# Optimization experiments

Measured on AMD Instinct MI355X. Metric: run time of the kernel, lower is better.

The kernel has to match this reference:

```python
import jax, jax.numpy as jnp
import numpy as np

B, H, L, N = 16, 128, 4096, 64
DT_MIN, DT_MAX = 0.001, 0.1


def _make_dplr_hippo(n):
    # NPLR HiPPO -> DPLR diagonalization (numpy, init-time only)
    p0 = np.sqrt(1 + 2 * np.arange(n))
    A = p0[:, None] * p0[None, :]
    A = -(np.tril(A) - np.diag(np.arange(n)))
    p = np.sqrt(np.arange(n) + 0.5)
    b = np.sqrt(2 * np.arange(n) + 1.0)
    S = A + p[:, None] * p[None, :]
    Lam_re = np.mean(np.diagonal(S)) * np.ones(n)
    Lam_im, V = np.linalg.eigh(S * -1j)
    p = V.conj().T @ p
    b = V.conj().T @ b
    return Lam_re + 1j * Lam_im, p, b


def setup_inputs() -> dict:
    key = jax.random.key(0)
    k1, k2, k3 = jax.random.split(key, 3)
    Lam, p, b = _make_dplr_hippo(N)
    tile = lambda a: jnp.tile(jnp.asarray(a, jnp.float32)[None], (H, 1))
    Lambda_re = tile(Lam.real)
    Lambda_im = tile(Lam.imag)
    P_ri = jnp.tile(jnp.stack([jnp.asarray(p.real, jnp.float32), jnp.asarray(p.imag, jnp.float32)], -1)[None], (H, 1, 1))
    B_ri = jnp.tile(jnp.stack([jnp.asarray(b.real, jnp.float32), jnp.asarray(b.imag, jnp.float32)], -1)[None], (H, 1, 1))
    C = (0.5 ** 0.5) * jax.random.normal(k1, (H, N, 2), jnp.float32)
    log_step = jax.random.uniform(k2, (H,)) * (np.log(DT_MAX) - np.log(DT_MIN)) + np.log(DT_MIN)
    D = jnp.ones((H,), jnp.float32)
    u = jax.random.normal(k3, (B, H, L), jnp.float32)
    return {"u": u, "Lambda_re": Lambda_re, "Lambda_im": Lambda_im, "P_ri": P_ri,
            "B_ri": B_ri, "C": C, "log_step": log_step.astype(jnp.float32), "D": D}


def reference(u, Lambda_re, Lambda_im, P_ri, B_ri, C, log_step, D):
    Lseq = u.shape[-1]
    # setup(): Lambda = clip(Lambda_re, max=-1e-4) + i*Lambda_im ; C complex ; step = exp(log_step)
    Lam = jnp.minimum(Lambda_re, -1e-4) + 1j * Lambda_im            # [H,N]
    P = P_ri[..., 0] + 1j * P_ri[..., 1]                             # [H,N]
    Bm = B_ri[..., 0] + 1j * B_ri[..., 1]                            # [H,N]
    Cc = C[..., 0] + 1j * C[..., 1]                                  # [H,N]
    step = jnp.exp(log_step)                                         # [H]
    # kernel_DPLR at the roots of unity
    Omega = jnp.exp(-2j * jnp.pi * (jnp.arange(Lseq) / Lseq))        # [L]
    g = (2.0 / step)[:, None] * ((1.0 - Omega) / (1.0 + Omega))[None, :]  # [H,L]
    c = 2.0 / (1.0 + Omega)                                          # [L]
    den = 1.0 / (g[:, :, None] - Lam[:, None, :])                    # [H,L,N] resolvent
    # four Cauchy dot products, batched: v stacked on last axis
    Vmat = jnp.stack([Cc.conj() * Bm, Cc.conj() * P, P.conj() * Bm, P.conj() * P], axis=-1)  # [H,N,4]
    Ks = jnp.einsum('hln,hnk->hlk', den, Vmat)                       # [H,L,4]
    k00, k01, k10, k11 = Ks[..., 0], Ks[..., 1], Ks[..., 2], Ks[..., 3]
    atRoots = c[None, :] * (k00 - k01 * (1.0 / (1.0 + k11)) * k10)   # [H,L]
    K = jnp.fft.ifft(atRoots, Lseq, axis=-1).real                    # [H,L] SSM kernel
    # causal FFT convolution: pad both to 2L
    ud = jnp.fft.rfft(jnp.pad(u, ((0, 0), (0, 0), (0, Lseq))), axis=-1)   # [B,H,L+1]
    Kd = jnp.fft.rfft(jnp.pad(K, ((0, 0), (0, Lseq))), axis=-1)           # [H,L+1]
    y = jnp.fft.irfft(ud * Kd[None], axis=-1)[..., :Lseq]            # [B,H,L]
    return y + D[None, :, None] * u
```

## Files before the change

kernel.cpp:

```cpp
#include <hip/hip_runtime.h>
#include <hip/hip_bf16.h>


#define PI_F 3.14159265358979323846f

__device__ __forceinline__ float2 cmulf(float2 a, float2 b) {
  return make_float2(a.x * b.x - a.y * b.y, a.x * b.y + a.y * b.x);
}
__device__ __forceinline__ void cmul_set(float2& v, float wr, float wi) {
  v = make_float2(v.x * wr - v.y * wi, v.x * wi + v.y * wr);
}
__device__ __forceinline__ int ad(int k) { return k + (k >> 4); }

template <int SIGN>
__device__ __forceinline__ void bfly4(float2& a, float2& b, float2& c,
                                      float2& d) {
  float t0x = a.x + c.x, t0y = a.y + c.y;
  float t1x = a.x - c.x, t1y = a.y - c.y;
  float t2x = b.x + d.x, t2y = b.y + d.y;
  float t3x = b.x - d.x, t3y = b.y - d.y;
  a = make_float2(t0x + t2x, t0y + t2y);
  c = make_float2(t0x - t2x, t0y - t2y);
  if (SIGN < 0) {
    b = make_float2(t1x + t3y, t1y - t3x);
    d = make_float2(t1x - t3y, t1y + t3x);
  } else {
    b = make_float2(t1x - t3y, t1y + t3x);
    d = make_float2(t1x + t3y, t1y - t3x);
  }
}

template <int SIGN>
__device__ __forceinline__ void fft16(float2 v[16]) {
  const float sg = (float)SIGN;
  const float C1 = 0.92387953251128674f;
  const float S1 = 0.38268343236508978f;
  const float R2 = 0.70710678118654752f;
  bfly4<SIGN>(v[0], v[4], v[8], v[12]);
  bfly4<SIGN>(v[1], v[5], v[9], v[13]);
  bfly4<SIGN>(v[2], v[6], v[10], v[14]);
  bfly4<SIGN>(v[3], v[7], v[11], v[15]);
  cmul_set(v[5], C1, sg * S1);
  cmul_set(v[6], R2, sg * R2);
  cmul_set(v[7], S1, sg * C1);
  cmul_set(v[9], R2, sg * R2);
  v[10] = make_float2(-sg * v[10].y, sg * v[10].x);
  cmul_set(v[11], -R2, sg * R2);
  cmul_set(v[13], S1, sg * C1);
  cmul_set(v[14], -R2, sg * R2);
  cmul_set(v[15], -C1, -sg * S1);
  float2 w[16];
#pragma unroll
  for (int g = 0; g < 4; ++g) {
    float2 x0 = v[4 * g], x1 = v[4 * g + 1], x2 = v[4 * g + 2],
           x3 = v[4 * g + 3];
    bfly4<SIGN>(x0, x1, x2, x3);
    w[g] = x0; w[g + 4] = x1; w[g + 8] = x2; w[g + 12] = x3;
  }
#pragma unroll
  for (int i = 0; i < 16; ++i) v[i] = w[i];
}

template <int SIGN>
__device__ void fft4096_regs(float2 v[16], float2* lds, int tid) {
  const float TH1 = (float)SIGN * (2.0f * PI_F / 4096.0f);
  const float TH2 = (float)SIGN * (2.0f * PI_F / 256.0f);
  fft16<SIGN>(v);
  {
    float sn, cn;
    __sincosf(TH1 * (float)tid, &sn, &cn);
    float2 w1 = make_float2(cn, sn), cw = w1;
#pragma unroll
    for (int g = 1; g < 16; ++g) {
      v[g] = cmulf(v[g], cw);
      if (g < 15) cw = cmulf(cw, w1);
    }
  }
  __syncthreads();
#pragma unroll
  for (int g = 0; g < 16; ++g) lds[tid * 17 + g] = v[g];
  __syncthreads();
  const int a = tid & 15, g2 = tid >> 4;
#pragma unroll
  for (int b = 0; b < 16; ++b) v[b] = lds[a * 17 + b * 272 + g2];
  fft16<SIGN>(v);
  {
    float sn, cn;
    __sincosf(TH2 * (float)a, &sn, &cn);
    float2 w1 = make_float2(cn, sn), cw = w1;
#pragma unroll
    for (int b = 1; b < 16; ++b) {
      v[b] = cmulf(v[b], cw);
      if (b < 15) cw = cmulf(cw, w1);
    }
  }
  __syncthreads();
#pragma unroll
  for (int b = 0; b < 16; ++b) lds[g2 * 17 + b * 273 + a] = v[b];
  __syncthreads();
#pragma unroll
  for (int a2 = 0; a2 < 16; ++a2) v[a2] = lds[g2 * 17 + a * 273 + a2];
  fft16<SIGN>(v);
}

__global__ __launch_bounds__(256) void k_cauchy(
    const float* __restrict__ Lre, const float* __restrict__ Lim,
    const float* __restrict__ Pri, const float* __restrict__ Bri,
    const float* __restrict__ Cri, const float* __restrict__ lstep,
    float2* __restrict__ atR) {
  __shared__ float4 pA[64];
  __shared__ float4 pB[64];
  __shared__ float2 pL[64];
  const int h = blockIdx.x >> 2;
  const int sub = blockIdx.x & 3;
  const int tid = threadIdx.x;
  if (tid < 64) {
    int n = tid;
    int base = h * 64 + n;
    float lr = fminf(Lre[base], -1e-4f);
    float li = Lim[base];
    float pr = Pri[2 * base], pi = Pri[2 * base + 1];
    float br = Bri[2 * base], bi = Bri[2 * base + 1];
    float cr = Cri[2 * base], ci = Cri[2 * base + 1];
    pA[n] = make_float4(cr * br + ci * bi, cr * bi - ci * br,
                        cr * pr + ci * pi, cr * pi - ci * pr);
    pB[n] = make_float4(pr * br + pi * bi, pr * bi - pi * br,
                        pr * pr + pi * pi, 0.f);
    pL[n] = make_float2(lr, li);
  }
  __syncthreads();
  const float istep = expf(-lstep[h]);

  float trm[4], tim[4], qrm[4], qim[4];
#pragma unroll
  for (int i = 0; i < 4; ++i) {
    int m = sub * 1024 + i * 256 + tid;
    float ang = -(2.0f * PI_F / 4096.0f) * (float)m;
    float sn, cn;
    __sincosf(ang, &sn, &cn);
    trm[i] = 0.5f * (1.0f + cn);
    tim[i] = 0.5f * sn;
    qrm[i] = (1.0f - cn) * istep;
    qim[i] = -sn * istep;
  }
  float S[4][8];
#pragma unroll
  for (int i = 0; i < 4; ++i)
#pragma unroll
    for (int jj = 0; jj < 8; ++jj) S[i][jj] = 0.f;

#pragma unroll 4
  for (int n = 0; n < 64; ++n) {
    float4 a = pA[n];
    float4 b = pB[n];
    float2 L = pL[n];
#pragma unroll
    for (int i = 0; i < 4; ++i) {
      float dr = qrm[i] - (trm[i] * L.x - tim[i] * L.y);
      float di = qim[i] - (trm[i] * L.y + tim[i] * L.x);
      float inv = __builtin_amdgcn_rcpf(dr * dr + di * di);
      float sr = dr * inv, si = -di * inv;
      S[i][0] += a.x * sr - a.y * si;  S[i][1] += a.x * si + a.y * sr;
      S[i][2] += a.z * sr - a.w * si;  S[i][3] += a.z * si + a.w * sr;
      S[i][4] += b.x * sr - b.y * si;  S[i][5] += b.x * si + b.y * sr;
      S[i][6] += b.z * sr;             S[i][7] += b.z * si;
    }
  }
#pragma unroll
  for (int i = 0; i < 4; ++i) {
    int m = sub * 1024 + i * 256 + tid;
    float tS11r = trm[i] * S[i][6] - tim[i] * S[i][7];
    float tS11i = trm[i] * S[i][7] + tim[i] * S[i][6];
    float denr = 1.0f + tS11r, deni = tS11i;
    float dinv = 1.0f / (denr * denr + deni * deni);
    float P1r = S[i][2] * S[i][4] - S[i][3] * S[i][5];
    float P1i = S[i][2] * S[i][5] + S[i][3] * S[i][4];
    float P2r = trm[i] * P1r - tim[i] * P1i;
    float P2i = trm[i] * P1i + tim[i] * P1r;
    float Qr = (P2r * denr + P2i * deni) * dinv;
    float Qi = (P2i * denr - P2r * deni) * dinv;
    atR[h * 4096 + m] = make_float2(S[i][0] - Qr, S[i][1] - Qi);
  }
}

__global__ __launch_bounds__(256) void k_khat(const float2* __restrict__ atR,
                                              const float* __restrict__ Dp,
                                              float2* __restrict__ Khat) {
  __shared__ float2 lds[4368];
  const int h = blockIdx.x;
  const int tid = threadIdx.x;
  float2 v[16];
#pragma unroll
  for (int c = 0; c < 16; ++c) v[c] = atR[h * 4096 + tid + 256 * c];
  fft4096_regs<1>(v, lds, tid);
  const int kb = (tid >> 4) + 16 * (tid & 15);
  float* ldsf = (float*)lds;
  const float s = 1.0f / 4096.0f;
  __syncthreads();
#pragma unroll
  for (int al = 0; al < 16; ++al) {
    int l = kb + 256 * al;
    ldsf[ad(l)] = v[al].x * s;
  }
  __syncthreads();
#pragma unroll
  for (int c = 0; c < 8; ++c) {
    int n = tid + 256 * c;
    v[c] = make_float2(ldsf[ad(2 * n)], ldsf[ad(2 * n + 1)]);
  }
#pragma unroll
  for (int c = 8; c < 16; ++c) v[c] = make_float2(0.f, 0.f);
  fft4096_regs<-1>(v, lds, tid);
  __syncthreads();
#pragma unroll
  for (int al = 0; al < 16; ++al) {
    int k = kb + 256 * al;
    lds[ad(k)] = v[al];
  }
  __syncthreads();
  const float Dh = Dp[h];
  float2* Kr = Khat + h * 4097;
  for (int k = tid; k <= 2048; k += 256) {
    float2 Zk = lds[ad(k)];
    float2 Zm = lds[ad((4096 - k) & 4095)];
    float Er = 0.5f * (Zk.x + Zm.x), Ei = 0.5f * (Zk.y - Zm.y);
    float Or = 0.5f * (Zk.y + Zm.y), Oi = 0.5f * (Zm.x - Zk.x);
    float swn, cwn;
    __sincosf(-(PI_F / 4096.0f) * (float)k, &swn, &cwn);
    float WOr = cwn * Or - swn * Oi, WOi = cwn * Oi + swn * Or;
    Kr[k] = make_float2(Er + WOr + Dh, Ei + WOi);
    if (k != 2048) Kr[4096 - k] = make_float2(Er - WOr + Dh, WOi - Ei);
  }
}

__global__ __launch_bounds__(256) void k_conv(const float* __restrict__ u,
                                              const float2* __restrict__ Khat,
                                              float* __restrict__ y) {
  __shared__ float2 lds[4368];
  const int r = blockIdx.x;
  const int h = r & 127;
  const int tid = threadIdx.x;
  const float2* u2 = (const float2*)(u + (size_t)r * 4096);
  float2 v[16];
#pragma unroll
  for (int c = 0; c < 8; ++c) v[c] = u2[tid + 256 * c];
#pragma unroll
  for (int c = 8; c < 16; ++c) v[c] = make_float2(0.f, 0.f);
  fft4096_regs<-1>(v, lds, tid);
  const int kb = (tid >> 4) + 16 * (tid & 15);
  __syncthreads();
#pragma unroll
  for (int al = 0; al < 16; ++al) {
    int k = kb + 256 * al;
    lds[ad(k)] = v[al];
  }
  __syncthreads();
  const float2* __restrict__ Kr = Khat + h * 4097;
  const float s = 1.0f / 4096.0f;
  for (int k = tid; k <= 2048; k += 256) {
    float2 Zk = lds[ad(k)];
    float2 Zm = lds[ad((4096 - k) & 4095)];
    float Er = 0.5f * (Zk.x + Zm.x), Ei = 0.5f * (Zk.y - Zm.y);
    float Or = 0.5f * (Zk.y + Zm.y), Oi = 0.5f * (Zm.x - Zk.x);
    float swn, cwn;
    __sincosf(-(PI_F / 4096.0f) * (float)k, &swn, &cwn);
    float WOr = cwn * Or - swn * Oi, WOi = cwn * Oi + swn * Or;
    float U1r = Er + WOr, U1i = Ei + WOi;
    float U2r = Er - WOr, U2i = WOi - Ei;
    float2 K1 = Kr[k], K2 = Kr[4096 - k];
    float Y1r = U1r * K1.x - U1i * K1.y, Y1i = U1r * K1.y + U1i * K1.x;
    float Y2r = U2r * K2.x - U2i * K2.y, Y2i = U2r * K2.y + U2i * K2.x;
    float Epr = 0.5f * (Y1r + Y2r), Epi = 0.5f * (Y1i - Y2i);
    float Tr = 0.5f * (Y1r - Y2r), Ti = 0.5f * (Y1i + Y2i);
    float O2r = cwn * Tr + swn * Ti, O2i = cwn * Ti - swn * Tr;
    lds[ad(k)] = make_float2((Epr - O2i) * s, (Epi + O2r) * s);
    if (k != 0 && k != 2048)
      lds[ad(4096 - k)] = make_float2((Epr + O2i) * s, (O2r - Epi) * s);
  }
  __syncthreads();
#pragma unroll
  for (int c = 0; c < 16; ++c) {
    int j = tid + 256 * c;
    v[c] = lds[ad(j)];
  }
  fft4096_regs<1>(v, lds, tid);
  __syncthreads();
#pragma unroll
  for (int al = 0; al < 8; ++al) {
    int k = kb + 256 * al;
    lds[ad(k)] = v[al];
  }
  __syncthreads();
  float4* y4 = (float4*)(y + (size_t)r * 4096);
#pragma unroll
  for (int i = 0; i < 4; ++i) {
    int j4 = tid + 256 * i;
    float2 z0 = lds[ad(2 * j4)];
    float2 z1 = lds[ad(2 * j4 + 1)];
    y4[j4] = make_float4(z0.x, z0.y, z1.x, z1.y);
  }
}

extern "C" void kernel_launch(void* const* d_in, const int* in_sizes, int n_in,
                              void* d_out, int out_size, void* d_ws,
                              size_t ws_size, hipStream_t stream) {
  (void)in_sizes; (void)n_in; (void)out_size; (void)ws_size;
  const float* u = (const float*)d_in[0];
  const float* Lre = (const float*)d_in[1];
  const float* Lim = (const float*)d_in[2];
  const float* Pri = (const float*)d_in[3];
  const float* Bri = (const float*)d_in[4];
  const float* Cri = (const float*)d_in[5];
  const float* lst = (const float*)d_in[6];
  const float* Dp = (const float*)d_in[7];
  float* y = (float*)d_out;
  float2* atR = (float2*)d_ws;
  float2* Khat = (float2*)((char*)d_ws + (size_t)128 * 4096 * sizeof(float2));

  k_cauchy<<<512, 256, 0, stream>>>(Lre, Lim, Pri, Bri, Cri, lst, atR);
  k_khat<<<128, 256, 0, stream>>>(atR, Dp, Khat);
  k_conv<<<2048, 256, 0, stream>>>(u, Khat, y);
}
```

Baseline: 160.0 us.

## Fold rfft post-processing into precomputed spectral coefficients and skip bit-reversal reorders

k_khat now precomputes, per head, a pair of complex coefficients that fold the kernel spectrum, D term, real-FFT split twiddles and 1/L scale into one linear map on Z[k] and Z[-k]. k_conv applies that map directly in digit-reversed order and then runs a new scrambled-to-natural inverse FFT. This removes the separate split/recombine pass, one LDS reorder and the output reorder. The Cauchy kernel is spread over 4x more blocks with one frequency per thread, and launch bounds are added. In exchange the coefficient table is twice the size (float4 per bin) and more global traffic is read per conv block.

```diff
diff --git a/kernel.cpp b/kernel.cpp
--- a/kernel.cpp
+++ b/kernel.cpp
@@ -61,45 +61,58 @@
   for (int i = 0; i < 16; ++i) v[i] = w[i];
 }
 
+__device__ __forceinline__ void tw_apply(float2 v[16], float ang) {
+  float sn, cn;
+  __sincosf(ang, &sn, &cn);
+  float2 w1 = make_float2(cn, sn), cw = w1;
+#pragma unroll
+  for (int g = 1; g < 16; ++g) {
+    v[g] = cmulf(v[g], cw);
+    if (g < 15) cw = cmulf(cw, w1);
+  }
+}
+
 template <int SIGN>
 __device__ void fft4096_regs(float2 v[16], float2* lds, int tid) {
-  const float TH1 = (float)SIGN * (2.0f * PI_F / 4096.0f);
-  const float TH2 = (float)SIGN * (2.0f * PI_F / 256.0f);
-  fft16<SIGN>(v);
-  {
-    float sn, cn;
-    __sincosf(TH1 * (float)tid, &sn, &cn);
-    float2 w1 = make_float2(cn, sn), cw = w1;
-#pragma unroll
-    for (int g = 1; g < 16; ++g) {
-      v[g] = cmulf(v[g], cw);
-      if (g < 15) cw = cmulf(cw, w1);
-    }
-  }
+  const int a = tid & 15, g2 = tid >> 4;
+  fft16<SIGN>(v);
+  tw_apply(v, (float)SIGN * (2.0f * PI_F / 4096.0f) * (float)tid);
   __syncthreads();
 #pragma unroll
   for (int g = 0; g < 16; ++g) lds[tid * 17 + g] = v[g];
   __syncthreads();
+#pragma unroll
+  for (int b = 0; b < 16; ++b) v[b] = lds[a * 17 + b * 272 + g2];
+  fft16<SIGN>(v);
+  tw_apply(v, (float)SIGN * (2.0f * PI_F / 256.0f) * (float)a);
+  __syncthreads();
+#pragma unroll
+  for (int b = 0; b < 16; ++b) lds[g2 * 17 + b * 273 + a] = v[b];
+  __syncthreads();
+#pragma unroll
+  for (int a2 = 0; a2 < 16; ++a2) v[a2] = lds[g2 * 17 + a * 273 + a2];
+  fft16<SIGN>(v);
+}
+
+template <int SIGN>
+__device__ void fft4096_scr2nat(float2 v[16], float2* lds, int tid) {
   const int a = tid & 15, g2 = tid >> 4;
-#pragma unroll
-  for (int b = 0; b < 16; ++b) v[b] = lds[a * 17 + b * 272 + g2];
-  fft16<SIGN>(v);
-  {
-    float sn, cn;
-    __sincosf(TH2 * (float)a, &sn, &cn);
-    float2 w1 = make_float2(cn, sn), cw = w1;
-#pragma unroll
-    for (int b = 1; b < 16; ++b) {
-      v[b] = cmulf(v[b], cw);
-      if (b < 15) cw = cmulf(cw, w1);
-    }
-  }
-  __syncthreads();
-#pragma unroll
-  for (int b = 0; b < 16; ++b) lds[g2 * 17 + b * 273 + a] = v[b];
-  __syncthreads();
-#pragma unroll
-  for (int a2 = 0; a2 < 16; ++a2) v[a2] = lds[g2 * 17 + a * 273 + a2];
+  fft16<SIGN>(v);
+  __syncthreads();
+#pragma unroll
+  for (int r = 0; r < 16; ++r) lds[g2 * 17 + a * 273 + r] = v[r];
+  __syncthreads();
+#pragma unroll
+  for (int b = 0; b < 16; ++b) v[b] = lds[g2 * 17 + b * 273 + a];
+  tw_apply(v, (float)SIGN * (2.0f * PI_F / 256.0f) * (float)a);
+  fft16<SIGN>(v);
+  __syncthreads();
+#pragma unroll
+  for (int r = 0; r < 16; ++r) lds[272 * r + 17 * a + g2] = v[r];
+  __syncthreads();
+#pragma unroll
+  for (int g = 0; g < 16; ++g) v[g] = lds[tid * 17 + g];
+  tw_apply(v, (float)SIGN * (2.0f * PI_F / 4096.0f) * (float)tid);
   fft16<SIGN>(v);
 }
 
@@ -111,81 +124,63 @@
   __shared__ float4 pA[64];
   __shared__ float4 pB[64];
   __shared__ float2 pL[64];
-  const int h = blockIdx.x >> 2;
-  const int sub = blockIdx.x & 3;
+  const int h = blockIdx.x >> 4;
+  const int sub = blockIdx.x & 15;
   const int tid = threadIdx.x;
   if (tid < 64) {
-    int n = tid;
-    int base = h * 64 + n;
+    int base = h * 64 + tid;
     float lr = fminf(Lre[base], -1e-4f);
     float li = Lim[base];
     float pr = Pri[2 * base], pi = Pri[2 * base + 1];
     float br = Bri[2 * base], bi = Bri[2 * base + 1];
     float cr = Cri[2 * base], ci = Cri[2 * base + 1];
-    pA[n] = make_float4(cr * br + ci * bi, cr * bi - ci * br,
-                        cr * pr + ci * pi, cr * pi - ci * pr);
-    pB[n] = make_float4(pr * br + pi * bi, pr * bi - pi * br,
-                        pr * pr + pi * pi, 0.f);
-    pL[n] = make_float2(lr, li);
+    pA[tid] = make_float4(cr * br + ci * bi, cr * bi - ci * br,
+                          cr * pr + ci * pi, cr * pi - ci * pr);
+    pB[tid] = make_float4(pr * br + pi * bi, pr * bi - pi * br,
+                          pr * pr + pi * pi, 0.f);
+    pL[tid] = make_float2(lr, li);
   }
   __syncthreads();
   const float istep = expf(-lstep[h]);
-
-  float trm[4], tim[4], qrm[4], qim[4];
-#pragma unroll
-  for (int i = 0; i < 4; ++i) {
-    int m = sub * 1024 + i * 256 + tid;
-    float ang = -(2.0f * PI_F / 4096.0f) * (float)m;
-    float sn, cn;
-    __sincosf(ang, &sn, &cn);
-    trm[i] = 0.5f * (1.0f + cn);
-    tim[i] = 0.5f * sn;
-    qrm[i] = (1.0f - cn) * istep;
-    qim[i] = -sn * istep;
-  }
-  float S[4][8];
-#pragma unroll
-  for (int i = 0; i < 4; ++i)
-#pragma unroll
-    for (int jj = 0; jj < 8; ++jj) S[i][jj] = 0.f;
-
-#pragma unroll 4
+  const int m = sub * 256 + tid;
+  float sn, cn;
+  __sincosf(-(2.0f * PI_F / 4096.0f) * (float)m, &sn, &cn);
+  const float trm = 0.5f * (1.0f + cn);
+  const float tim = 0.5f * sn;
+  const float qrm = (1.0f - cn) * istep;
+  const float qim = -sn * istep;
+  float S0 = 0.f, S1 = 0.f, S2 = 0.f, S3 = 0.f, S4 = 0.f, S5 = 0.f, S6 = 0.f,
+        S7 = 0.f;
+#pragma unroll 8
   for (int n = 0; n < 64; ++n) {
     float4 a = pA[n];
     float4 b = pB[n];
     float2 L = pL[n];
-#pragma unroll
-    for (int i = 0; i < 4; ++i) {
-      float dr = qrm[i] - (trm[i] * L.x - tim[i] * L.y);
-      float di = qim[i] - (trm[i] * L.y + tim[i] * L.x);
-      float inv = __builtin_amdgcn_rcpf(dr * dr + di * di);
-      float sr = dr * inv, si = -di * inv;
-      S[i][0] += a.x * sr - a.y * si;  S[i][1] += a.x * si + a.y * sr;
-      S[i][2] += a.z * sr - a.w * si;  S[i][3] += a.z * si + a.w * sr;
-      S[i][4] += b.x * sr - b.y * si;  S[i][5] += b.x * si + b.y * sr;
-      S[i][6] += b.z * sr;             S[i][7] += b.z * si;
-    }
-  }
-#pragma unroll
-  for (int i = 0; i < 4; ++i) {
-    int m = sub * 1024 + i * 256 + tid;
-    float tS11r = trm[i] * S[i][6] - tim[i] * S[i][7];
-    float tS11i = trm[i] * S[i][7] + tim[i] * S[i][6];
-    float denr = 1.0f + tS11r, deni = tS11i;
-    float dinv = 1.0f / (denr * denr + deni * deni);
-    float P1r = S[i][2] * S[i][4] - S[i][3] * S[i][5];
-    float P1i = S[i][2] * S[i][5] + S[i][3] * S[i][4];
-    float P2r = trm[i] * P1r - tim[i] * P1i;
-    float P2i = trm[i] * P1i + tim[i] * P1r;
-    float Qr = (P2r * denr + P2i * deni) * dinv;
-    float Qi = (P2i * denr - P2r * deni) * dinv;
-    atR[h * 4096 + m] = make_float2(S[i][0] - Qr, S[i][1] - Qi);
-  }
-}
-
-__global__ __launch_bounds__(256) void k_khat(const float2* __restrict__ atR,
-                                              const float* __restrict__ Dp,
-                                              float2* __restrict__ Khat) {
+    float dr = qrm - (trm * L.x - tim * L.y);
+    float di = qim - (trm * L.y + tim * L.x);
+    float inv = __builtin_amdgcn_rcpf(dr * dr + di * di);
+    float sr = dr * inv, si = -di * inv;
+    S0 += a.x * sr - a.y * si;  S1 += a.x * si + a.y * sr;
+    S2 += a.z * sr - a.w * si;  S3 += a.z * si + a.w * sr;
+    S4 += b.x * sr - b.y * si;  S5 += b.x * si + b.y * sr;
+    S6 += b.z * sr;             S7 += b.z * si;
+  }
+  float tS11r = trm * S6 - tim * S7;
+  float tS11i = trm * S7 + tim * S6;
+  float denr = 1.0f + tS11r, deni = tS11i;
+  float dinv = 1.0f / (denr * denr + deni * deni);
+  float P1r = S2 * S4 - S3 * S5;
+  float P1i = S2 * S5 + S3 * S4;
+  float P2r = trm * P1r - tim * P1i;
+  float P2i = trm * P1i + tim * P1r;
+  float Qr = (P2r * denr + P2i * deni) * dinv;
+  float Qi = (P2i * denr - P2r * deni) * dinv;
+  atR[h * 4096 + m] = make_float2(S0 - Qr, S1 - Qi);
+}
+
+__global__ __launch_bounds__(256, 4) void k_khat(
+    const float2* __restrict__ atR, const float* __restrict__ Dp,
+    float4* __restrict__ abt) {
   __shared__ float2 lds[4368];
   const int h = blockIdx.x;
   const int tid = threadIdx.x;
@@ -198,10 +193,7 @@
   const float s = 1.0f / 4096.0f;
   __syncthreads();
 #pragma unroll
-  for (int al = 0; al < 16; ++al) {
-    int l = kb + 256 * al;
-    ldsf[ad(l)] = v[al].x * s;
-  }
+  for (int al = 0; al < 16; ++al) ldsf[ad(kb + 256 * al)] = v[al].x * s;
   __syncthreads();
 #pragma unroll
   for (int c = 0; c < 8; ++c) {
@@ -213,29 +205,30 @@
   fft4096_regs<-1>(v, lds, tid);
   __syncthreads();
 #pragma unroll
-  for (int al = 0; al < 16; ++al) {
-    int k = kb + 256 * al;
-    lds[ad(k)] = v[al];
-  }
+  for (int al = 0; al < 16; ++al) lds[ad(kb + 256 * al)] = v[al];
   __syncthreads();
   const float Dh = Dp[h];
-  float2* Kr = Khat + h * 4097;
-  for (int k = tid; k <= 2048; k += 256) {
+#pragma unroll
+  for (int c = 0; c < 16; ++c) {
+    int k = kb + 256 * c;
     float2 Zk = lds[ad(k)];
     float2 Zm = lds[ad((4096 - k) & 4095)];
     float Er = 0.5f * (Zk.x + Zm.x), Ei = 0.5f * (Zk.y - Zm.y);
     float Or = 0.5f * (Zk.y + Zm.y), Oi = 0.5f * (Zm.x - Zk.x);
-    float swn, cwn;
-    __sincosf(-(PI_F / 4096.0f) * (float)k, &swn, &cwn);
-    float WOr = cwn * Or - swn * Oi, WOi = cwn * Oi + swn * Or;
-    Kr[k] = make_float2(Er + WOr + Dh, Ei + WOi);
-    if (k != 2048) Kr[4096 - k] = make_float2(Er - WOr + Dh, WOi - Ei);
-  }
-}
-
-__global__ __launch_bounds__(256) void k_conv(const float* __restrict__ u,
-                                              const float2* __restrict__ Khat,
-                                              float* __restrict__ y) {
+    float s_, c_;
+    __sincosf(-(PI_F / 4096.0f) * (float)k, &s_, &c_);
+    float Gr = c_ * Or - s_ * Oi, Gi = c_ * Oi + s_ * Or;
+    float ar = (Er + Dh + s_ * Gr) * s;
+    float ai = (Ei + s_ * Gi) * s;
+    float br = (-c_ * Gi) * s;
+    float bi = (c_ * Gr) * s;
+    abt[h * 4096 + tid + 256 * c] = make_float4(ar, ai, br, bi);
+  }
+}
+
+__global__ __launch_bounds__(256, 4) void k_conv(const float* __restrict__ u,
+                                                 const float4* __restrict__ abt,
+                                                 float* __restrict__ y) {
   __shared__ float2 lds[4368];
   const int r = blockIdx.x;
   const int h = r & 127;
@@ -250,55 +243,22 @@
   const int kb = (tid >> 4) + 16 * (tid & 15);
   __syncthreads();
 #pragma unroll
+  for (int al = 0; al < 16; ++al) lds[ad(kb + 256 * al)] = v[al];
+  __syncthreads();
+  const float4* __restrict__ abrow = abt + h * 4096;
+#pragma unroll
   for (int al = 0; al < 16; ++al) {
     int k = kb + 256 * al;
-    lds[ad(k)] = v[al];
-  }
-  __syncthreads();
-  const float2* __restrict__ Kr = Khat + h * 4097;
-  const float s = 1.0f / 4096.0f;
-  for (int k = tid; k <= 2048; k += 256) {
-    float2 Zk = lds[ad(k)];
+    float4 ab = abrow[tid + 256 * al];
     float2 Zm = lds[ad((4096 - k) & 4095)];
-    float Er = 0.5f * (Zk.x + Zm.x), Ei = 0.5f * (Zk.y - Zm.y);
-    float Or = 0.5f * (Zk.y + Zm.y), Oi = 0.5f * (Zm.x - Zk.x);
-    float swn, cwn;
-    __sincosf(-(PI_F / 4096.0f) * (float)k, &swn, &cwn);
-    float WOr = cwn * Or - swn * Oi, WOi = cwn * Oi + swn * Or;
-    float U1r = Er + WOr, U1i = Ei + WOi;
-    float U2r = Er - WOr, U2i = WOi - Ei;
-    float2 K1 = Kr[k], K2 = Kr[4096 - k];
-    float Y1r = U1r * K1.x - U1i * K1.y, Y1i = U1r * K1.y + U1i * K1.x;
-    float Y2r = U2r * K2.x - U2i * K2.y, Y2i = U2r * K2.y + U2i * K2.x;
-    float Epr = 0.5f * (Y1r + Y2r), Epi = 0.5f * (Y1i - Y2i);
-    float Tr = 0.5f * (Y1r - Y2r), Ti = 0.5f * (Y1i + Y2i);
-    float O2r = cwn * Tr + swn * Ti, O2i = cwn * Ti - swn * Tr;
-    lds[ad(k)] = make_float2((Epr - O2i) * s, (Epi + O2r) * s);
-    if (k != 0 && k != 2048)
-      lds[ad(4096 - k)] = make_float2((Epr + O2i) * s, (O2r - Epi) * s);
-  }
-  __syncthreads();
-#pragma unroll
-  for (int c = 0; c < 16; ++c) {
-    int j = tid + 256 * c;
-    v[c] = lds[ad(j)];
-  }
-  fft4096_regs<1>(v, lds, tid);
-  __syncthreads();
-#pragma unroll
-  for (int al = 0; al < 8; ++al) {
-    int k = kb + 256 * al;
-    lds[ad(k)] = v[al];
-  }
-  __syncthreads();
-  float4* y4 = (float4*)(y + (size_t)r * 4096);
-#pragma unroll
-  for (int i = 0; i < 4; ++i) {
-    int j4 = tid + 256 * i;
-    float2 z0 = lds[ad(2 * j4)];
-    float2 z1 = lds[ad(2 * j4 + 1)];
-    y4[j4] = make_float4(z0.x, z0.y, z1.x, z1.y);
-  }
+    float2 Zk = v[al];
+    v[al] = make_float2(ab.x * Zk.x - ab.y * Zk.y + ab.z * Zm.x + ab.w * Zm.y,
+                        ab.x * Zk.y + ab.y * Zk.x + ab.w * Zm.x - ab.z * Zm.y);
+  }
+  fft4096_scr2nat<1>(v, lds, tid);
+  float2* y2 = (float2*)(y + (size_t)r * 4096);
+#pragma unroll
+  for (int c = 0; c < 8; ++c) y2[tid + 256 * c] = v[c];
 }
 
 extern "C" void kernel_launch(void* const* d_in, const int* in_sizes, int n_in,
@@ -315,9 +275,9 @@
   const float* Dp = (const float*)d_in[7];
   float* y = (float*)d_out;
   float2* atR = (float2*)d_ws;
-  float2* Khat = (float2*)((char*)d_ws + (size_t)128 * 4096 * sizeof(float2));
-
-  k_cauchy<<<512, 256, 0, stream>>>(Lre, Lim, Pri, Bri, Cri, lst, atR);
-  k_khat<<<128, 256, 0, stream>>>(atR, Dp, Khat);
-  k_conv<<<2048, 256, 0, stream>>>(u, Khat, y);
-}
+  float4* abt = (float4*)((char*)d_ws + (size_t)4 * 1024 * 1024);
+
+  k_cauchy<<<2048, 256, 0, stream>>>(Lre, Lim, Pri, Bri, Cri, lst, atR);
+  k_khat<<<128, 256, 0, stream>>>(atR, Dp, abt);
+  k_conv<<<2048, 256, 0, stream>>>(u, abt, y);
+}
```

Measured after the change: 161.0 us. Within noise of the previous version (+0.6%).
